# Optimization experiments

Hardware: AMD Instinct MI355X
Metric: run time of the kernel (lower is better)

The kernel has to match this reference:

```python
import jax, jax.numpy as jnp
import numpy as np

C, K, N = 128, 27, 4096   # channels, kernel offsets (3^3), parent points
M = 8 * N                  # child points (FCG: up to 8 children per parent)


def sp_conv(f, nbr, W):
    # sparse submanifold conv: gather K neighbors then per-offset GEMM
    # f: [P, C], nbr: [P, K], W: [K, C, C] -> [P, C]
    return jnp.einsum('pkc,kcd->pd', f[nbr], W)


def resnet(f, nbr, Wa, Wb):
    h = jax.nn.relu(sp_conv(f, nbr, Wa))
    return jax.nn.relu(sp_conv(h, nbr, Wb) + f)


def setup_inputs():
    key = jax.random.key(0)
    ks = jax.random.split(key, 30)
    conv = lambda k: jax.random.normal(k, (K, C, C), dtype=jnp.float32) * 0.02
    return {
        'x_O': jax.random.randint(ks[0], (N,), 0, 256, dtype=jnp.int32),
        'gt_O': jax.random.randint(ks[1], (M, 1), 0, 256, dtype=jnp.int32),
        'nbr_par': jax.random.randint(ks[2], (N, K), 0, N, dtype=jnp.int32),
        'nbr_child': jax.random.randint(ks[3], (M, K), 0, M, dtype=jnp.int32),
        'child_oct': jnp.tile(jnp.arange(8, dtype=jnp.int32), N),
        'prior_emb': jax.random.normal(ks[4], (256, C), dtype=jnp.float32),
        'pW0': conv(ks[5]), 'pW1a': conv(ks[6]), 'pW1b': conv(ks[7]),
        'pW2a': conv(ks[8]), 'pW2b': conv(ks[9]),
        'oct_emb': jax.random.normal(ks[10], (8, C), dtype=jnp.float32) * 0.1,
        'tW0': conv(ks[11]), 'tW1a': conv(ks[12]), 'tW1b': conv(ks[13]),
        'tW2a': conv(ks[14]), 'tW2b': conv(ks[15]),
        's1_emb': jax.random.normal(ks[16], (16, C), dtype=jnp.float32) * 0.1,
        'h0W1': jax.random.normal(ks[17], (C, C), dtype=jnp.float32) * 0.09,
        'h0b1': jnp.zeros((C,), dtype=jnp.float32),
        'h0W2': jax.random.normal(ks[18], (C, 16), dtype=jnp.float32) * 0.09,
        'h0b2': jnp.zeros((16,), dtype=jnp.float32),
        'h1W1': jax.random.normal(ks[19], (C, C), dtype=jnp.float32) * 0.09,
        'h1b1': jnp.zeros((C,), dtype=jnp.float32),
        'h1W2': jax.random.normal(ks[20], (C, 16), dtype=jnp.float32) * 0.09,
        'h1b2': jnp.zeros((16,), dtype=jnp.float32),
    }


def reference(x_O, gt_O, nbr_par, nbr_child, child_oct,
              prior_emb, pW0, pW1a, pW1b, pW2a, pW2b,
              oct_emb, tW0, tW1a, tW1b, tW2a, tW2b, s1_emb,
              h0W1, h0b1, h0W2, h0b2, h1W1, h1b1, h1W2, h1b2):
    # prior branch: occupancy byte embedding + sparse ResNet stack
    f = prior_emb[x_O]                                   # [N, C]
    f = jax.nn.relu(sp_conv(f, nbr_par, pW0))
    f = resnet(f, nbr_par, pW1a, pW1b)
    f = resnet(f, nbr_par, pW2a, pW2b)
    # FCG: broadcast parent feature to its 8 children; TargetEmbedding adds octant embedding
    g = jnp.repeat(f, 8, axis=0) + oct_emb[child_oct]    # [M, C]
    g = jax.nn.relu(sp_conv(g, nbr_child, tW0))
    g = resnet(g, nbr_child, tW1a, tW1b)
    g = resnet(g, nbr_child, tW2a, tW2b)
    # two-stage 4-bit occupancy prediction + gather-based entropy
    gt_s0 = jnp.remainder(gt_O, 16)                      # [M, 1]
    gt_s1 = gt_O // 16
    p0 = jax.nn.softmax(jax.nn.relu(g @ h0W1 + h0b1) @ h0W2 + h0b2, axis=-1)
    g1 = g + s1_emb[gt_s0[:, 0]]
    p1 = jax.nn.softmax(jax.nn.relu(g1 @ h1W1 + h1b1) @ h1W2 + h1b2, axis=-1)
    b0 = jnp.take_along_axis(p0, gt_s0, axis=1)
    b1 = jnp.take_along_axis(p1, gt_s1, axis=1)
    bits = (jnp.sum(jnp.clip(-jnp.log2(b0 + 1e-10), 0.0, 50.0))
            + jnp.sum(jnp.clip(-jnp.log2(b1 + 1e-10), 0.0, 50.0)))
    return bits / jnp.float32(N)
```

## Files before the change

kernel.cpp:

```cpp
#include <hip/hip_runtime.h>

typedef unsigned int u32;
typedef unsigned short u16;
typedef short bf16x8 __attribute__((ext_vector_type(8)));
typedef float f32x4 __attribute__((ext_vector_type(4)));
typedef unsigned short u16x4 __attribute__((ext_vector_type(4)));

#define KOFF 27

__device__ __forceinline__ float bf2f(u16 u) {
    u32 x = ((u32)u) << 16;
    return __builtin_bit_cast(float, x);
}
__device__ __forceinline__ u16 f2bf(float f) {
    u32 u = __builtin_bit_cast(u32, f);
    u32 r = (u + 0x7FFFu + ((u >> 16) & 1u)) >> 16;
    return (u16)r;
}
__device__ __forceinline__ void async16(void* lds, const void* g) {
    __builtin_amdgcn_global_load_lds(
        (const __attribute__((address_space(1))) u32*)g,
        (__attribute__((address_space(3))) u32*)lds, 16, 0, 0);
}

struct PrepArgs {
    const float* ws[12];
    u16* wd[12];
    const float* h0W2;
    const float* h1W2;
    u16* wt2h;
    const float* s1emb;
    const float* h1W1f;
    float* E1;
};
__global__ __launch_bounds__(256) void prep_mega(PrepArgs a) {
    __shared__ float t[128][65];
    const int bid = blockIdx.x;
    if (bid < 544) {
        int w, k, half;
        if (bid < 540) {
            w = bid / 54;
            int r = bid % 54;
            k = r >> 1;
            half = r & 1;
        } else {
            int r = bid - 540;
            w = 10 + (r >> 1);
            k = 0;
            half = r & 1;
        }
        const float* s = a.ws[w] + k * 16384 + half * 64;
        for (int i = threadIdx.x; i < 8192; i += 256) {
            int c = i >> 6, dl = i & 63;
            t[c][dl] = s[c * 128 + dl];
        }
        __syncthreads();
        u16* db = a.wd[w] + k * 16384;
        for (int i = threadIdx.x; i < 8192; i += 256) {
            int dl = i >> 7, c = i & 127;
            int d = half * 64 + dl;
            db[d * 128 + (c ^ ((d & 7) << 3))] = f2bf(t[c][dl]);
        }
    } else if (bid < 546) {
        int h = bid - 544;
        const float* src = h ? a.h1W2 : a.h0W2;
        u16* dst = a.wt2h + h * 2048;
        for (int i = threadIdx.x; i < 2048; i += 256) {
            int j = i >> 7, d = i & 127;
            dst[j * 128 + (d ^ ((j & 7) << 3))] = f2bf(src[d * 16 + j]);
        }
    } else {
        int b = bid - 546;
        int r = b * 2 + (threadIdx.x >> 7);
        int c = threadIdx.x & 127;
        float acc = 0.f;
        for (int kx = 0; kx < 128; ++kx)
            acc = fmaf(a.s1emb[r * 128 + kx], a.h1W1f[kx * 128 + c], acc);
        a.E1[r * 128 + c] = acc;
    }
}

__global__ __launch_bounds__(256) void embed_k(const int* __restrict__ xO,
                                               const float* __restrict__ emb,
                                               u16* __restrict__ out) {
    int idx = blockIdx.x * 256 + threadIdx.x;
    int c = idx & 127, n = idx >> 7;
    out[idx] = f2bf(emb[xO[n] * 128 + c]);
}

__global__ __launch_bounds__(256) void expand_k(const u16* __restrict__ f,
                                                const int* __restrict__ oct,
                                                const float* __restrict__ oemb,
                                                u16* __restrict__ g) {
    int idx = blockIdx.x * 256 + threadIdx.x;
    int c = idx & 127, m = idx >> 7;
    g[idx] = f2bf(bf2f(f[(m >> 3) * 128 + c]) + oemb[oct[m] * 128 + c]);
}

template <bool PARTIAL>
__global__ __launch_bounds__(256, 2) void conv2(
    const u16* __restrict__ fin, const int* __restrict__ nbr,
    const u16* __restrict__ wt, const u16* __restrict__ res,
    u16* __restrict__ fout, float* __restrict__ pout, int npts) {
    constexpr int BM = 64;
    __shared__ __align__(16) u16 Asb[2][BM * 128];
    __shared__ __align__(16) u16 Bsb[128 * 128];
    __shared__ int nbrS[BM * KOFF];
    const int tid = threadIdx.x;
    const int wid = tid >> 6;
    const int lane = tid & 63;
    const int p0 = blockIdx.x * BM;
    const int g = PARTIAL ? blockIdx.y : 0;
    const int k0 = PARTIAL ? (g * KOFF) >> 3 : 0;
    const int k1 = PARTIAL ? ((g + 1) * KOFF) >> 3 : KOFF;

    for (int i = tid; i < BM * KOFF; i += 256)
        nbrS[i] = nbr[(p0 + i / KOFF) * KOFF + (i % KOFF)];
    __syncthreads();

    f32x4 acc[2][4];
#pragma unroll
    for (int m = 0; m < 2; ++m)
#pragma unroll
        for (int n = 0; n < 4; ++n) acc[m][n] = f32x4{0.f, 0.f, 0.f, 0.f};

    const int RB = (wid >> 1) * 32;
    const int CB = (wid & 1) * 64;
    const int lrow = lane & 15;
    const int lkb = (lane >> 4) * 16;

    auto stageA = [&](int k, int buf) {
#pragma unroll
        for (int i = 0; i < 4; ++i) {
            int o = i * 4096 + tid * 16;
            int r = o >> 8;
            int cbs = (o & 255) ^ ((r & 7) << 4);
            int rg = nbrS[r * KOFF + k];
            async16((char*)&Asb[buf][0] + i * 4096 + wid * 1024,
                    (const char*)fin + (size_t)rg * 256 + cbs);
        }
    };
    auto stageB = [&](int k) {
        const char* wk = (const char*)wt + k * 32768;
#pragma unroll
        for (int i = 0; i < 8; ++i)
            async16((char*)&Bsb[0] + i * 4096 + wid * 1024,
                    wk + i * 4096 + tid * 16);
    };

    stageA(k0, 0);
    int cur = 0;
#pragma unroll 1
    for (int k = k0; k < k1; ++k) {
        __builtin_amdgcn_s_barrier();
        stageB(k);
        if (k + 1 < k1) {
            stageA(k + 1, cur ^ 1);
            asm volatile("s_waitcnt vmcnt(4)" ::: "memory");
        } else {
            asm volatile("s_waitcnt vmcnt(0)" ::: "memory");
        }
        __builtin_amdgcn_s_barrier();
        __builtin_amdgcn_sched_barrier(0);
        __builtin_amdgcn_s_setprio(1);
#pragma unroll
        for (int kk = 0; kk < 4; ++kk) {
            bf16x8 av[2], bv[4];
#pragma unroll
            for (int m = 0; m < 2; ++m) {
                int row = RB + m * 16 + lrow;
                int cb = (kk * 64 + lkb) ^ ((row & 7) << 4);
                av[m] = *(const bf16x8*)((const char*)&Asb[cur][0] + row * 256 + cb);
            }
#pragma unroll
            for (int n = 0; n < 4; ++n) {
                int drow = CB + n * 16 + lrow;
                int cb = (kk * 64 + lkb) ^ ((drow & 7) << 4);
                bv[n] = *(const bf16x8*)((const char*)&Bsb[0] + drow * 256 + cb);
            }
#pragma unroll
            for (int m = 0; m < 2; ++m)
#pragma unroll
                for (int n = 0; n < 4; ++n)
                    acc[m][n] = __builtin_amdgcn_mfma_f32_16x16x32_bf16(
                        av[m], bv[n], acc[m][n], 0, 0, 0);
        }
        __builtin_amdgcn_s_setprio(0);
        cur ^= 1;
    }

    if constexpr (PARTIAL) {
        float* pg = pout + (size_t)g * npts * 128;
#pragma unroll
        for (int m = 0; m < 2; ++m) {
            int prow = p0 + RB + m * 16 + (lane >> 4) * 4;
#pragma unroll
            for (int n = 0; n < 4; ++n) {
                int dcol = CB + n * 16 + lrow;
#pragma unroll
                for (int q = 0; q < 4; ++q)
                    pg[(prow + q) * 128 + dcol] = acc[m][n][q];
            }
        }
    } else {
#pragma unroll
        for (int m = 0; m < 2; ++m) {
            int prow = p0 + RB + m * 16 + (lane >> 4) * 4;
#pragma unroll
            for (int n = 0; n < 4; ++n) {
                int dcol = CB + n * 16 + lrow;
#pragma unroll
                for (int q = 0; q < 4; ++q) {
                    float v = acc[m][n][q];
                    int p = prow + q;
                    if (res) v += bf2f(res[p * 128 + dcol]);
                    v = v > 0.f ? v : 0.f;
                    fout[p * 128 + dcol] = f2bf(v);
                }
            }
        }
    }
}

__global__ __launch_bounds__(256) void combine_k(const float* __restrict__ P,
                                                 const u16* __restrict__ res,
                                                 u16* __restrict__ fout,
                                                 int nelem) {
    int base = (blockIdx.x * 256 + threadIdx.x) * 4;
    f32x4 s = *(const f32x4*)(P + base);
#pragma unroll
    for (int gg = 1; gg < 8; ++gg)
        s += *(const f32x4*)(P + (size_t)gg * nelem + base);
    u16x4 o;
    if (res) {
        u16x4 rv = *(const u16x4*)(res + base);
#pragma unroll
        for (int j = 0; j < 4; ++j) s[j] += bf2f(rv[j]);
    }
#pragma unroll
    for (int j = 0; j < 4; ++j) {
        float v = s[j] > 0.f ? s[j] : 0.f;
        o[j] = f2bf(v);
    }
    *(u16x4*)(fout + base) = o;
}

__global__ __launch_bounds__(512, 1) void fused_heads(
    const u16* __restrict__ G, const int* __restrict__ gtO,
    const u16* __restrict__ wt2, const u16* __restrict__ wt2h,
    const float* __restrict__ b1a, const float* __restrict__ b1b,
    const float* __restrict__ E1, const float* __restrict__ b2a,
    const float* __restrict__ b2b, float* __restrict__ partial) {
    __shared__ __align__(16) u16 AB[49152];
    __shared__ __align__(16) u16 W2ts[4096];
    __shared__ float E1s[2048];
    __shared__ float b2s[32];
    __shared__ int gts[256];
    __shared__ float bitsS[256];
    u16* Asb = AB;
    u16* Bsb = AB + 16384;
    char* Hb = (char*)AB;
    const int tid = threadIdx.x, wid = tid >> 6, lane = tid & 63;
    const int lrow = lane & 15, lkb = (lane >> 4) * 16;
    const int p0 = blockIdx.x * 128;

#pragma unroll
    for (int i = 0; i < 4; ++i) {
        int o = i * 8192 + tid * 16;
        int r = o >> 8;
        int cbs = (o & 255) ^ ((r & 7) << 4);
        async16((char*)Asb + i * 8192 + wid * 1024,
                (const char*)G + (size_t)(p0 + r) * 256 + cbs);
    }
#pragma unroll
    for (int i = 0; i < 8; ++i)
        async16((char*)Bsb + i * 8192 + wid * 1024,
                (const char*)wt2 + i * 8192 + tid * 16);
    async16((char*)W2ts + wid * 1024, (const char*)wt2h + tid * 16);
    for (int i = tid; i < 2048; i += 512) E1s[i] = E1[i];
    if (tid < 16) b2s[tid] = b2a[tid];
    else if (tid < 32) b2s[tid] = b2b[tid - 16];
    if (tid < 128) {
        int g = gtO[p0 + tid];
        gts[tid] = g & 15;
        gts[128 + tid] = g >> 4;
    }
    __syncthreads();

    const int RB = (wid >> 1) * 32, CB = (wid & 1) * 128;
    f32x4 acc[2][8];
#pragma unroll
    for (int m = 0; m < 2; ++m)
#pragma unroll
        for (int n = 0; n < 8; ++n) acc[m][n] = f32x4{0.f, 0.f, 0.f, 0.f};
    __builtin_amdgcn_s_setprio(1);
#pragma unroll
    for (int kk = 0; kk < 4; ++kk) {
        bf16x8 av[2], bv[8];
#pragma unroll
        for (int m = 0; m < 2; ++m) {
            int row = RB + m * 16 + lrow;
            int cb = (kk * 64 + lkb) ^ ((row & 7) << 4);
            av[m] = *(const bf16x8*)((const char*)Asb + row * 256 + cb);
        }
#pragma unroll
        for (int n = 0; n < 8; ++n) {
            int drow = CB + n * 16 + lrow;
            int cb = (kk * 64 + lkb) ^ ((drow & 7) << 4);
            bv[n] = *(const bf16x8*)((const char*)Bsb + drow * 256 + cb);
        }
#pragma unroll
        for (int m = 0; m < 2; ++m)
#pragma unroll
            for (int n = 0; n < 8; ++n)
                acc[m][n] = __builtin_amdgcn_mfma_f32_16x16x32_bf16(
                    av[m], bv[n], acc[m][n], 0, 0, 0);
    }
    __builtin_amdgcn_s_setprio(0);
    __syncthreads();

    const float* b1p = CB ? b1b : b1a;
    float b1v[8];
#pragma unroll
    for (int n = 0; n < 8; ++n) b1v[n] = b1p[n * 16 + lrow];
#pragma unroll
    for (int m = 0; m < 2; ++m) {
#pragma unroll
        for (int q = 0; q < 4; ++q) {
            int p = RB + m * 16 + (lane >> 4) * 4 + q;
#pragma unroll
            for (int n = 0; n < 8; ++n) {
                float v = acc[m][n][q] + b1v[n];
                if (CB) v += E1s[gts[p] * 128 + n * 16 + lrow];
                v = v > 0.f ? v : 0.f;
                int colb = (CB + n * 16 + lrow) * 2;
                *(u16*)(Hb + p * 512 + (colb ^ ((p & 7) << 4))) = f2bf(v);
            }
        }
    }
    __syncthreads();

    const int RB2 = wid * 16;
    f32x4 acc2[2];
    acc2[0] = f32x4{0.f, 0.f, 0.f, 0.f};
    acc2[1] = f32x4{0.f, 0.f, 0.f, 0.f};
#pragma unroll
    for (int kk = 0; kk < 4; ++kk) {
        int row = RB2 + lrow;
        int cb = (kk * 64 + lkb) ^ ((row & 7) << 4);
        int cbw = (kk * 64 + lkb) ^ ((lrow & 7) << 4);
#pragma unroll
        for (int h = 0; h < 2; ++h) {
            bf16x8 a2 = *(const bf16x8*)(Hb + row * 512 + h * 256 + cb);
            bf16x8 b2v = *(const bf16x8*)((const char*)W2ts + h * 4096 +
                                          lrow * 256 + cbw);
            acc2[h] = __builtin_amdgcn_mfma_f32_16x16x32_bf16(a2, b2v, acc2[h],
                                                              0, 0, 0);
        }
    }
    const int jj = lrow;
#pragma unroll
    for (int h = 0; h < 2; ++h) {
#pragma unroll
        for (int q = 0; q < 4; ++q) {
            int pt = RB2 + (lane >> 4) * 4 + q;
            float v = acc2[h][q] + b2s[h * 16 + jj];
            float mx = v;
#pragma unroll
            for (int o = 1; o < 16; o <<= 1) mx = fmaxf(mx, __shfl_xor(mx, o, 16));
            float e = expf(v - mx);
            float s = e;
#pragma unroll
            for (int o = 1; o < 16; o <<= 1) s += __shfl_xor(s, o, 16);
            float bits = -log2f(e / s + 1e-10f);
            bits = fminf(fmaxf(bits, 0.f), 50.f);
            if (jj == gts[h * 128 + pt]) bitsS[h * 128 + pt] = bits;
        }
    }
    __syncthreads();
    if (tid < 64) {
        float s = bitsS[tid] + bitsS[tid + 64] + bitsS[tid + 128] + bitsS[tid + 192];
#pragma unroll
        for (int o = 32; o > 0; o >>= 1) s += __shfl_down(s, o, 64);
        if (tid == 0) partial[blockIdx.x] = s;
    }
}

__global__ __launch_bounds__(256) void finalize_k(const float* __restrict__ partial,
                                                  float* __restrict__ out, int n) {
    float s = 0.f;
    for (int i = threadIdx.x; i < n; i += 256) s += partial[i];
#pragma unroll
    for (int o = 32; o > 0; o >>= 1) s += __shfl_down(s, o, 64);
    __shared__ float wsum[4];
    if ((threadIdx.x & 63) == 0) wsum[threadIdx.x >> 6] = s;
    __syncthreads();
    if (threadIdx.x == 0)
        out[0] = (wsum[0] + wsum[1] + wsum[2] + wsum[3]) * (1.0f / 4096.0f);
}

extern "C" void kernel_launch(void* const* d_in, const int* in_sizes, int n_in,
                              void* d_out, int out_size, void* d_ws,
                              size_t ws_size, hipStream_t stream) {
    const int N = 4096, M = 32768;
    const int* x_O = (const int*)d_in[0];
    const int* gt_O = (const int*)d_in[1];
    const int* nbr_par = (const int*)d_in[2];
    const int* nbr_ch = (const int*)d_in[3];
    const int* child_oct = (const int*)d_in[4];
    const float* prior_emb = (const float*)d_in[5];
    const float* convW[10] = {
        (const float*)d_in[6],  (const float*)d_in[7],  (const float*)d_in[8],
        (const float*)d_in[9],  (const float*)d_in[10], (const float*)d_in[12],
        (const float*)d_in[13], (const float*)d_in[14], (const float*)d_in[15],
        (const float*)d_in[16]};
    const float* oct_emb = (const float*)d_in[11];
    const float* s1_emb = (const float*)d_in[17];
    const float* h0W1 = (const float*)d_in[18];
    const float* h0b1 = (const float*)d_in[19];
    const float* h0W2 = (const float*)d_in[20];
    const float* h0b2 = (const float*)d_in[21];
    const float* h1W1 = (const float*)d_in[22];
    const float* h1b1 = (const float*)d_in[23];
    const float* h1W2 = (const float*)d_in[24];
    const float* h1b2 = (const float*)d_in[25];

    char* ws = (char*)d_ws;
    size_t off = 0;
    auto alloc = [&](size_t b) {
        void* p = ws + off;
        off += (b + 255) & ~(size_t)255;
        return p;
    };
    PrepArgs pa;
    for (int i = 0; i < 10; ++i) {
        pa.ws[i] = convW[i];
        pa.wd[i] = (u16*)alloc(27 * 128 * 128 * 2);
    }
    u16* Wt2 = (u16*)alloc(256 * 128 * 2);
    pa.ws[10] = h0W1;
    pa.ws[11] = h1W1;
    pa.wd[10] = Wt2;
    pa.wd[11] = Wt2 + 128 * 128;
    u16* wt2h = (u16*)alloc(2 * 16 * 128 * 2);
    float* E1 = (float*)alloc(16 * 128 * 4);
    pa.h0W2 = h0W2;
    pa.h1W2 = h1W2;
    pa.wt2h = wt2h;
    pa.s1emb = s1_emb;
    pa.h1W1f = h1W1;
    pa.E1 = E1;

    u16* fA = (u16*)alloc((size_t)N * 256);
    u16* fB = (u16*)alloc((size_t)N * 256);
    u16* fC = (u16*)alloc((size_t)N * 256);
    u16* gA = (u16*)alloc((size_t)M * 256);
    u16* gB = (u16*)alloc((size_t)M * 256);
    u16* gC = (u16*)alloc((size_t)M * 256);
    float* partial = (float*)alloc(256 * 4);
    float* pconv = (float*)gA;

    prep_mega<<<554, 256, 0, stream>>>(pa);
    embed_k<<<N * 128 / 256, 256, 0, stream>>>(x_O, prior_emb, fA);

    const int PE = N * 128;
    conv2<true><<<dim3(64, 8), 256, 0, stream>>>(fA, nbr_par, pa.wd[0], nullptr, nullptr, pconv, N);
    combine_k<<<PE / 1024, 256, 0, stream>>>(pconv, nullptr, fB, PE);
    conv2<true><<<dim3(64, 8), 256, 0, stream>>>(fB, nbr_par, pa.wd[1], nullptr, nullptr, pconv, N);
    combine_k<<<PE / 1024, 256, 0, stream>>>(pconv, nullptr, fC, PE);
    conv2<true><<<dim3(64, 8), 256, 0, stream>>>(fC, nbr_par, pa.wd[2], nullptr, nullptr, pconv, N);
    combine_k<<<PE / 1024, 256, 0, stream>>>(pconv, fB, fA, PE);
    conv2<true><<<dim3(64, 8), 256, 0, stream>>>(fA, nbr_par, pa.wd[3], nullptr, nullptr, pconv, N);
    combine_k<<<PE / 1024, 256, 0, stream>>>(pconv, nullptr, fC, PE);
    conv2<true><<<dim3(64, 8), 256, 0, stream>>>(fC, nbr_par, pa.wd[4], nullptr, nullptr, pconv, N);
    combine_k<<<PE / 1024, 256, 0, stream>>>(pconv, fA, fB, PE);

    expand_k<<<M * 128 / 256, 256, 0, stream>>>(fB, child_oct, oct_emb, gA);

    conv2<false><<<dim3(512, 1), 256, 0, stream>>>(gA, nbr_ch, pa.wd[5], nullptr, gB, nullptr, M);
    conv2<false><<<dim3(512, 1), 256, 0, stream>>>(gB, nbr_ch, pa.wd[6], nullptr, gC, nullptr, M);
    conv2<false><<<dim3(512, 1), 256, 0, stream>>>(gC, nbr_ch, pa.wd[7], gB, gA, nullptr, M);
    conv2<false><<<dim3(512, 1), 256, 0, stream>>>(gA, nbr_ch, pa.wd[8], nullptr, gC, nullptr, M);
    conv2<false><<<dim3(512, 1), 256, 0, stream>>>(gC, nbr_ch, pa.wd[9], gA, gB, nullptr, M);

    fused_heads<<<M / 128, 512, 0, stream>>>(gB, gt_O, Wt2, wt2h, h0b1, h1b1,
                                             E1, h0b2, h1b2, partial);
    finalize_k<<<1, 256, 0, stream>>>(partial, (float*)d_out, 256);

    (void)in_sizes; (void)n_in; (void)out_size; (void)ws_size;
}
```

Measured before the change: 339.6 us.

## Load conv weights directly into registers with double-buffered prefetch, drop LDS B tile

The per-offset weight tile is no longer staged through shared memory. Each wave now loads its B fragments straight from global memory into two register buffers, prefetching the next offset while the current one feeds the MFMAs, and the loop is unrolled by two to alternate the buffers. This removes the 32KB LDS B buffer and its reads, and the shared-memory reuse of weights across waves. In exchange it adds a large register cost (two sets of 16 bf16x8 vectors, about 128 VGPRs), duplicates global weight loads across waves, and depends on hand-tuned vmcnt counts.

```diff
diff --git a/kernel.cpp b/kernel.cpp
--- a/kernel.cpp
+++ b/kernel.cpp
@@ -98,13 +98,12 @@
 }
 
 template <bool PARTIAL>
-__global__ __launch_bounds__(256, 2) void conv2(
+__global__ __launch_bounds__(256, 2) void conv3(
     const u16* __restrict__ fin, const int* __restrict__ nbr,
     const u16* __restrict__ wt, const u16* __restrict__ res,
     u16* __restrict__ fout, float* __restrict__ pout, int npts) {
     constexpr int BM = 64;
     __shared__ __align__(16) u16 Asb[2][BM * 128];
-    __shared__ __align__(16) u16 Bsb[128 * 128];
     __shared__ int nbrS[BM * KOFF];
     const int tid = threadIdx.x;
     const int wid = tid >> 6;
@@ -140,23 +139,34 @@
                     (const char*)fin + (size_t)rg * 256 + cbs);
         }
     };
-    auto stageB = [&](int k) {
+    auto loadB = [&](int k, bf16x8 (&B)[16]) {
         const char* wk = (const char*)wt + k * 32768;
 #pragma unroll
-        for (int i = 0; i < 8; ++i)
-            async16((char*)&Bsb[0] + i * 4096 + wid * 1024,
-                    wk + i * 4096 + tid * 16);
+        for (int n = 0; n < 4; ++n) {
+            int drow = CB + n * 16 + lrow;
+            const char* rowp = wk + drow * 256;
+#pragma unroll
+            for (int kk = 0; kk < 4; ++kk) {
+                int cb = (kk * 64 + lkb) ^ ((drow & 7) << 4);
+                asm volatile("global_load_dwordx4 %0, %1, off"
+                             : "=&v"(B[n * 4 + kk])
+                             : "v"(rowp + cb)
+                             : "memory");
+            }
+        }
     };
 
+    bf16x8 brA[16], brB[16];
     stageA(k0, 0);
-    int cur = 0;
-#pragma unroll 1
-    for (int k = k0; k < k1; ++k) {
+    loadB(k0, brA);
+
+    auto body = [&](bf16x8 (&Bc)[16], bf16x8 (&Bn)[16], int k) {
+        const int ab = (k - k0) & 1;
         __builtin_amdgcn_s_barrier();
-        stageB(k);
         if (k + 1 < k1) {
-            stageA(k + 1, cur ^ 1);
-            asm volatile("s_waitcnt vmcnt(4)" ::: "memory");
+            stageA(k + 1, ab ^ 1);
+            loadB(k + 1, Bn);
+            asm volatile("s_waitcnt vmcnt(20)" ::: "memory");
         } else {
             asm volatile("s_waitcnt vmcnt(0)" ::: "memory");
         }
@@ -165,28 +175,29 @@
         __builtin_amdgcn_s_setprio(1);
 #pragma unroll
         for (int kk = 0; kk < 4; ++kk) {
-            bf16x8 av[2], bv[4];
+            bf16x8 av[2];
 #pragma unroll
             for (int m = 0; m < 2; ++m) {
                 int row = RB + m * 16 + lrow;
                 int cb = (kk * 64 + lkb) ^ ((row & 7) << 4);
-                av[m] = *(const bf16x8*)((const char*)&Asb[cur][0] + row * 256 + cb);
-            }
-#pragma unroll
-            for (int n = 0; n < 4; ++n) {
-                int drow = CB + n * 16 + lrow;
-                int cb = (kk * 64 + lkb) ^ ((drow & 7) << 4);
-                bv[n] = *(const bf16x8*)((const char*)&Bsb[0] + drow * 256 + cb);
+                av[m] = *(const bf16x8*)((const char*)&Asb[ab][0] + row * 256 + cb);
             }
 #pragma unroll
             for (int m = 0; m < 2; ++m)
 #pragma unroll
                 for (int n = 0; n < 4; ++n)
                     acc[m][n] = __builtin_amdgcn_mfma_f32_16x16x32_bf16(
-                        av[m], bv[n], acc[m][n], 0, 0, 0);
+                        av[m], Bc[n * 4 + kk], acc[m][n], 0, 0, 0);
         }
         __builtin_amdgcn_s_setprio(0);
-        cur ^= 1;
+    };
+
+    int k = k0;
+    while (true) {
+        body(brA, brB, k);
+        if (++k >= k1) break;
+        body(brB, brA, k);
+        if (++k >= k1) break;
     }
 
     if constexpr (PARTIAL) {
@@ -464,24 +475,24 @@
     embed_k<<<N * 128 / 256, 256, 0, stream>>>(x_O, prior_emb, fA);
 
     const int PE = N * 128;
-    conv2<true><<<dim3(64, 8), 256, 0, stream>>>(fA, nbr_par, pa.wd[0], nullptr, nullptr, pconv, N);
+    conv3<true><<<dim3(64, 8), 256, 0, stream>>>(fA, nbr_par, pa.wd[0], nullptr, nullptr, pconv, N);
     combine_k<<<PE / 1024, 256, 0, stream>>>(pconv, nullptr, fB, PE);
-    conv2<true><<<dim3(64, 8), 256, 0, stream>>>(fB, nbr_par, pa.wd[1], nullptr, nullptr, pconv, N);
+    conv3<true><<<dim3(64, 8), 256, 0, stream>>>(fB, nbr_par, pa.wd[1], nullptr, nullptr, pconv, N);
     combine_k<<<PE / 1024, 256, 0, stream>>>(pconv, nullptr, fC, PE);
-    conv2<true><<<dim3(64, 8), 256, 0, stream>>>(fC, nbr_par, pa.wd[2], nullptr, nullptr, pconv, N);
+    conv3<true><<<dim3(64, 8), 256, 0, stream>>>(fC, nbr_par, pa.wd[2], nullptr, nullptr, pconv, N);
     combine_k<<<PE / 1024, 256, 0, stream>>>(pconv, fB, fA, PE);
-    conv2<true><<<dim3(64, 8), 256, 0, stream>>>(fA, nbr_par, pa.wd[3], nullptr, nullptr, pconv, N);
+    conv3<true><<<dim3(64, 8), 256, 0, stream>>>(fA, nbr_par, pa.wd[3], nullptr, nullptr, pconv, N);
     combine_k<<<PE / 1024, 256, 0, stream>>>(pconv, nullptr, fC, PE);
-    conv2<true><<<dim3(64, 8), 256, 0, stream>>>(fC, nbr_par, pa.wd[4], nullptr, nullptr, pconv, N);
+    conv3<true><<<dim3(64, 8), 256, 0, stream>>>(fC, nbr_par, pa.wd[4], nullptr, nullptr, pconv, N);
     combine_k<<<PE / 1024, 256, 0, stream>>>(pconv, fA, fB, PE);
 
     expand_k<<<M * 128 / 256, 256, 0, stream>>>(fB, child_oct, oct_emb, gA);
 
-    conv2<false><<<dim3(512, 1), 256, 0, stream>>>(gA, nbr_ch, pa.wd[5], nullptr, gB, nullptr, M);
-    conv2<false><<<dim3(512, 1), 256, 0, stream>>>(gB, nbr_ch, pa.wd[6], nullptr, gC, nullptr, M);
-    conv2<false><<<dim3(512, 1), 256, 0, stream>>>(gC, nbr_ch, pa.wd[7], gB, gA, nullptr, M);
-    conv2<false><<<dim3(512, 1), 256, 0, stream>>>(gA, nbr_ch, pa.wd[8], nullptr, gC, nullptr, M);
-    conv2<false><<<dim3(512, 1), 256, 0, stream>>>(gC, nbr_ch, pa.wd[9], gA, gB, nullptr, M);
+    conv3<false><<<dim3(512, 1), 256, 0, stream>>>(gA, nbr_ch, pa.wd[5], nullptr, gB, nullptr, M);
+    conv3<false><<<dim3(512, 1), 256, 0, stream>>>(gB, nbr_ch, pa.wd[6], nullptr, gC, nullptr, M);
+    conv3<false><<<dim3(512, 1), 256, 0, stream>>>(gC, nbr_ch, pa.wd[7], gB, gA, nullptr, M);
+    conv3<false><<<dim3(512, 1), 256, 0, stream>>>(gA, nbr_ch, pa.wd[8], nullptr, gC, nullptr, M);
+    conv3<false><<<dim3(512, 1), 256, 0, stream>>>(gC, nbr_ch, pa.wd[9], gA, gB, nullptr, M);
 
     fused_heads<<<M / 128, 512, 0, stream>>>(gB, gt_O, Wt2, wt2h, h0b1, h1b1,
                                              E1, h0b2, h1b2, partial);
```

Result: slower. 430.7 us (+26.9%).
